# Kernel optimization log

Measured on AMD Instinct MI355X. Metric: run time of the kernel, lower is better.

The kernel has to match this reference:

```python
import jax, jax.numpy as jnp
import numpy as np

B, S, D = 4, 2048, 1024
E = 8
DFF = 4096
CAP_FACTOR = 1.25


def setup_inputs() -> dict:
    key = jax.random.key(0)
    ks = jax.random.split(key, 4)
    std_gate = float(np.sqrt(0.1 / D))
    inputs = jax.random.normal(ks[0], (B, S, D), dtype=jnp.float32)
    gate_w = jax.random.normal(ks[1], (E, D), dtype=jnp.float32) * std_gate
    w1 = jax.random.normal(ks[2], (E, D, DFF), dtype=jnp.float32) * (1.0 / np.sqrt(D))
    b1 = jnp.zeros((E, DFF), dtype=jnp.float32)
    w2 = jax.random.normal(ks[3], (E, DFF, D), dtype=jnp.float32) * (1.0 / np.sqrt(DFF))
    b2 = jnp.zeros((E, D), dtype=jnp.float32)
    return {"inputs": inputs, "gate_w": gate_w, "w1": w1, "b1": b1, "w2": w2, "b2": b2}


def reference(inputs, gate_w, w1, b1, w2, b2):
    d_model = inputs.shape[-1]
    tokens = inputs.reshape(-1, d_model)            # [T, D]
    T = tokens.shape[0]
    num_experts = gate_w.shape[0]
    capacity = int(np.ceil(CAP_FACTOR * T / num_experts))

    # fp32 gate (FP32LinearGate): logits = tokens @ gate_w.T
    logits = jnp.einsum('td,ed->te', tokens.astype(jnp.float32), gate_w)
    probs = jax.nn.softmax(logits, axis=-1)         # [T, E]

    # Top-1 routing with capacity
    expert_idx = jnp.argmax(probs, axis=-1)         # [T]
    mask = jax.nn.one_hot(expert_idx, num_experts, dtype=jnp.float32)  # [T, E]
    ranks = jnp.cumsum(mask, axis=0) - 1.0          # position of each token within its expert
    keep = (ranks < capacity) * mask                # drop tokens over capacity, [T, E]
    pos = ranks.astype(jnp.int32)                   # [T, E]
    # sec_mask: [T, E, C] one-hot placement of kept tokens into capacity slots
    sec_mask = jax.nn.one_hot(pos, capacity, dtype=jnp.float32) * keep[:, :, None]
    combine_weights = probs[:, :, None] * sec_mask  # [T, E, C]

    # Dispatch: dense matmul against routing mask (fallback path of MoeLayer)
    dispatch = jnp.einsum('tec,td->ecd', sec_mask, tokens)  # [E, C, D]

    # Grouped expert FFN
    h = jax.nn.relu(jnp.einsum('ecd,edh->ech', dispatch, w1) + b1[:, None, :])
    expert_out = jnp.einsum('ech,ehd->ecd', h, w2) + b2[:, None, :]  # [E, C, D]

    # Combine
    ans = jnp.einsum('tec,ecd->td', combine_weights, expert_out)
    return ans.reshape(inputs.shape)
```

## Files before the change

kernel.cpp:

```cpp
#include <hip/hip_runtime.h>
#include <hip/hip_bf16.h>

#define TOKENS 8192
#define DMODEL 1024
#define NEXP   8
#define DFF    4096
#define CAP    1280

typedef short bf16x8_t __attribute__((ext_vector_type(8)));
typedef float f32x4_t  __attribute__((ext_vector_type(4)));

__device__ __forceinline__ float bf2f(ushort u) {
    union { unsigned int i; float f; } v; v.i = ((unsigned int)u) << 16; return v.f;
}
__device__ __forceinline__ ushort f2bf(float f) {
    union { float f; unsigned int i; } v; v.f = f;
    unsigned int r = v.i + 0x7fffu + ((v.i >> 16) & 1u);
    return (ushort)(r >> 16);
}
__device__ __forceinline__ void load_lds16(const void* g, void* l) {
    __builtin_amdgcn_global_load_lds(
        (const __attribute__((address_space(1))) void*)g,
        (__attribute__((address_space(3))) void*)l, 16, 0, 0);
}

__global__ __launch_bounds__(256) void gate_kernel(
    const float* __restrict__ tokens, const float* __restrict__ gw,
    int* __restrict__ eidx, float* __restrict__ prob)
{
    int lane = threadIdx.x & 63;
    int wave = threadIdx.x >> 6;
    int t = blockIdx.x * 4 + wave;
    const float* tok = tokens + (long)t * DMODEL;
    float s[NEXP] = {0.f,0.f,0.f,0.f,0.f,0.f,0.f,0.f};
    #pragma unroll
    for (int c = 0; c < 4; c++) {
        int d = c * 256 + lane * 4;
        float4 x = *(const float4*)(tok + d);
        #pragma unroll
        for (int e = 0; e < NEXP; e++) {
            float4 g = *(const float4*)(gw + e * DMODEL + d);
            s[e] += x.x*g.x + x.y*g.y + x.z*g.z + x.w*g.w;
        }
    }
    #pragma unroll
    for (int e = 0; e < NEXP; e++) {
        #pragma unroll
        for (int off = 32; off > 0; off >>= 1) s[e] += __shfl_xor(s[e], off);
    }
    if (lane == 0) {
        float m = s[0]; int am = 0;
        #pragma unroll
        for (int e = 1; e < NEXP; e++) if (s[e] > m) { m = s[e]; am = e; }
        float sum = 0.f;
        #pragma unroll
        for (int e = 0; e < NEXP; e++) sum += expf(s[e] - m);
        eidx[t] = am;
        prob[t] = 1.0f / sum;
    }
}

__global__ __launch_bounds__(256) void route_scan(
    const int* __restrict__ eidx, int* __restrict__ pos)
{
    __shared__ int hist[256][NEXP];
    int tid = threadIdx.x;
    int base = tid * 32;
    #pragma unroll
    for (int e = 0; e < NEXP; e++) hist[tid][e] = 0;
    for (int i = 0; i < 32; i++) hist[tid][eidx[base + i]]++;
    __syncthreads();
    if (tid < NEXP) {
        int run = 0;
        for (int i = 0; i < 256; i++) { int v = hist[i][tid]; hist[i][tid] = run; run += v; }
    }
    __syncthreads();
    for (int i = 0; i < 32; i++) {
        int e = eidx[base + i];
        pos[base + i] = hist[tid][e]++;
    }
}

__global__ __launch_bounds__(256) void dispatch_gather(
    const float* __restrict__ tokens, const int* __restrict__ eidx,
    const int* __restrict__ pos, ushort* __restrict__ disp)
{
    int t = blockIdx.x;
    int p = pos[t];
    if (p >= CAP) return;
    int e = eidx[t];
    int d = threadIdx.x * 4;
    float4 v = *(const float4*)(tokens + (long)t * DMODEL + d);
    union { uint2 u; ushort h[4]; } o;
    o.h[0] = f2bf(v.x); o.h[1] = f2bf(v.y); o.h[2] = f2bf(v.z); o.h[3] = f2bf(v.w);
    *(uint2*)(disp + ((long)e * CAP + p) * DMODEL + d) = o.u;
}

__global__ __launch_bounds__(256) void transpose_f32_bf16(
    const float* __restrict__ in, ushort* __restrict__ out, int R, int C)
{
    __shared__ ushort tile[64][72];
    long base = (long)blockIdx.z * R * C;
    int r0 = blockIdx.y * 64, c0 = blockIdx.x * 64;
    int tid = threadIdx.x;
    int rr = tid >> 2;
    int cc = (tid & 3) * 16;
    const float* ip = in + base + (long)(r0 + rr) * C + (c0 + cc);
    #pragma unroll
    for (int q = 0; q < 4; q++) {
        float4 v = *(const float4*)(ip + q * 4);
        tile[cc + q*4 + 0][rr] = f2bf(v.x);
        tile[cc + q*4 + 1][rr] = f2bf(v.y);
        tile[cc + q*4 + 2][rr] = f2bf(v.z);
        tile[cc + q*4 + 3][rr] = f2bf(v.w);
    }
    __syncthreads();
    ushort* op = out + base + (long)(c0 + rr) * R + (r0 + cc);
    *(uint4*)op       = *(const uint4*)&tile[rr][cc];
    *(uint4*)(op + 8) = *(const uint4*)&tile[rr][cc + 8];
}

__global__ __launch_bounds__(256) void gemm_bt(
    const ushort* __restrict__ A, const ushort* __restrict__ B,
    const float* __restrict__ bias, ushort* __restrict__ C,
    int M, int N, int K, int do_relu,
    long sA, long sB, long sBias, long sC)
{
    A += blockIdx.z * sA; B += blockIdx.z * sB;
    bias += blockIdx.z * sBias; C += blockIdx.z * sC;

    __shared__ ushort As[128 * 64];
    __shared__ ushort Bs[128 * 64];

    int tid  = threadIdx.x;
    int lane = tid & 63, wave = tid >> 6;
    int wm = (wave >> 1) * 64, wn = (wave & 1) * 64;
    int fm = lane & 15;
    int q  = lane >> 4;
    int rx = fm & 7;
    int m0 = blockIdx.y * 128, n0 = blockIdx.x * 128;

    int srow = lane >> 3;
    int schk = (lane & 7) ^ srow;
    const ushort* Ag = A + (long)(m0 + 32*wave + srow) * K + schk * 8;
    const ushort* Bg = B + (long)(n0 + 32*wave + srow) * K + schk * 8;
    ushort* AsW = &As[(32*wave) * 64];
    ushort* BsW = &Bs[(32*wave) * 64];

    f32x4_t acc[4][4];
    #pragma unroll
    for (int i = 0; i < 4; i++)
        #pragma unroll
        for (int j = 0; j < 4; j++) acc[i][j] = (f32x4_t){0.f,0.f,0.f,0.f};

    for (int k0 = 0; k0 < K; k0 += 64) {
        #pragma unroll
        for (int t = 0; t < 4; t++) {
            load_lds16(Ag + (long)(8*t) * K + k0, AsW + (8*t) * 64);
            load_lds16(Bg + (long)(8*t) * K + k0, BsW + (8*t) * 64);
        }
        __syncthreads();
        #pragma unroll
        for (int kk = 0; kk < 64; kk += 32) {
            int l0 = (kk >> 3) + q;
            bf16x8_t af[4], bf[4];
            #pragma unroll
            for (int i = 0; i < 4; i++) {
                int r = wm + 16*i + fm;
                af[i] = *(const bf16x8_t*)&As[r * 64 + (l0 ^ rx) * 8];
            }
            #pragma unroll
            for (int j = 0; j < 4; j++) {
                int r = wn + 16*j + fm;
                bf[j] = *(const bf16x8_t*)&Bs[r * 64 + (l0 ^ rx) * 8];
            }
            #pragma unroll
            for (int i = 0; i < 4; i++)
                #pragma unroll
                for (int j = 0; j < 4; j++)
                    acc[i][j] = __builtin_amdgcn_mfma_f32_16x16x32_bf16(af[i], bf[j], acc[i][j], 0, 0, 0);
        }
        __syncthreads();
    }

    #pragma unroll
    for (int j = 0; j < 4; j++) {
        int col = n0 + wn + 16*j + fm;
        float bv = bias[col];
        #pragma unroll
        for (int i = 0; i < 4; i++) {
            int row = m0 + wm + 16*i + q * 4;
            #pragma unroll
            for (int r = 0; r < 4; r++) {
                float v = acc[i][j][r] + bv;
                if (do_relu) v = fmaxf(v, 0.f);
                C[(long)(row + r) * N + col] = f2bf(v);
            }
        }
    }
}

__global__ __launch_bounds__(256) void combine_kernel(
    const ushort* __restrict__ eo, const int* __restrict__ eidx,
    const int* __restrict__ pos, const float* __restrict__ prob,
    float* __restrict__ out)
{
    int t = blockIdx.x;
    int p = pos[t];
    int d = threadIdx.x * 4;
    float4 o;
    if (p < CAP) {
        int e = eidx[t];
        float w = prob[t];
        union { uint2 u; ushort h[4]; } v;
        v.u = *(const uint2*)(eo + ((long)e * CAP + p) * DMODEL + d);
        o.x = w * bf2f(v.h[0]);
        o.y = w * bf2f(v.h[1]);
        o.z = w * bf2f(v.h[2]);
        o.w = w * bf2f(v.h[3]);
    } else {
        o = (float4){0.f, 0.f, 0.f, 0.f};
    }
    *(float4*)(out + (long)t * DMODEL + d) = o;
}

extern "C" void kernel_launch(void* const* d_in, const int* in_sizes, int n_in,
                              void* d_out, int out_size, void* d_ws, size_t ws_size,
                              hipStream_t stream) {
    const float* tokens = (const float*)d_in[0];
    const float* gate_w = (const float*)d_in[1];
    const float* w1     = (const float*)d_in[2];
    const float* b1     = (const float*)d_in[3];
    const float* w2     = (const float*)d_in[4];
    const float* b2     = (const float*)d_in[5];
    float* outp = (float*)d_out;

    char* w = (char*)d_ws;
    ushort* w1T  = (ushort*)w; w += (size_t)NEXP * DFF * DMODEL * 2;
    ushort* w2T  = (ushort*)w; w += (size_t)NEXP * DMODEL * DFF * 2;
    ushort* disp = (ushort*)w; w += (size_t)NEXP * CAP * DMODEL * 2;
    ushort* h    = (ushort*)w; w += (size_t)NEXP * CAP * DFF * 2;
    ushort* eo   = (ushort*)w; w += (size_t)NEXP * CAP * DMODEL * 2;
    int*   eidx  = (int*)w;   w += TOKENS * 4;
    int*   pos   = (int*)w;   w += TOKENS * 4;
    float* prob  = (float*)w; w += TOKENS * 4;

    transpose_f32_bf16<<<dim3(DFF/64, DMODEL/64, NEXP), 256, 0, stream>>>(w1, w1T, DMODEL, DFF);
    transpose_f32_bf16<<<dim3(DMODEL/64, DFF/64, NEXP), 256, 0, stream>>>(w2, w2T, DFF, DMODEL);

    gate_kernel<<<TOKENS/4, 256, 0, stream>>>(tokens, gate_w, eidx, prob);
    route_scan<<<1, 256, 0, stream>>>(eidx, pos);
    dispatch_gather<<<TOKENS, 256, 0, stream>>>(tokens, eidx, pos, disp);

    gemm_bt<<<dim3(DFF/128, CAP/128, NEXP), 256, 0, stream>>>(
        disp, w1T, b1, h, CAP, DFF, DMODEL, 1,
        (long)CAP*DMODEL, (long)DFF*DMODEL, DFF, (long)CAP*DFF);
    gemm_bt<<<dim3(DMODEL/128, CAP/128, NEXP), 256, 0, stream>>>(
        h, w2T, b2, eo, CAP, DMODEL, DFF, 0,
        (long)CAP*DFF, (long)DMODEL*DFF, DMODEL, (long)CAP*DMODEL);

    combine_kernel<<<TOKENS, 256, 0, stream>>>(eo, eidx, pos, prob, outp);
}
```

Measured before the change: 584.2 us.

## Rewrite expert GEMM with 256x256 double-buffered tiles and workgroup swizzle

Replaces the 128x128 single-buffered grouped GEMM with a 256x256 tile, 512-thread kernel that double-buffers LDS, prefetches the next K-tile while computing in four phases with fine-grained vmcnt waits, and raises wave priority around MFMA blocks. It also remaps workgroup IDs in an XCD-aware swizzle for better L2 locality. The larger tile raises arithmetic intensity and reduces global traffic. In exchange it uses 128 KB of LDS and many accumulator registers, which limits occupancy. The grids also shrink (e.g. 4x5x8 for the second GEMM), which may underfill the CUs and leave a tail.

```diff
diff --git a/kernel.cpp b/kernel.cpp
--- a/kernel.cpp
+++ b/kernel.cpp
@@ -120,81 +120,136 @@
     *(uint4*)(op + 8) = *(const uint4*)&tile[rr][cc + 8];
 }
 
-__global__ __launch_bounds__(256) void gemm_bt(
+#define BM 256
+#define BN 256
+#define BK 64
+#define TILE_E (BM*BK)
+
+__global__ __launch_bounds__(512, 2) void gemm_bt256(
     const ushort* __restrict__ A, const ushort* __restrict__ B,
     const float* __restrict__ bias, ushort* __restrict__ C,
-    int M, int N, int K, int do_relu,
+    int N, int K, int do_relu,
     long sA, long sB, long sBias, long sC)
 {
-    A += blockIdx.z * sA; B += blockIdx.z * sB;
-    bias += blockIdx.z * sBias; C += blockIdx.z * sC;
-
-    __shared__ ushort As[128 * 64];
-    __shared__ ushort Bs[128 * 64];
+    __shared__ ushort As[2*TILE_E];
+    __shared__ ushort Bs[2*TILE_E];
+
+    int gx = gridDim.x, gy = gridDim.y;
+    int nwg = gx * gy * gridDim.z;
+    int lin = blockIdx.x + gx * (blockIdx.y + gy * blockIdx.z);
+    int cpx = nwg >> 3;
+    int swz = (lin & 7) * cpx + (lin >> 3);
+    int bz  = swz / (gx * gy);
+    int rem = swz - bz * gx * gy;
+    int by  = rem / gx, bx = rem - by * gx;
+
+    A += bz * sA; B += bz * sB; bias += bz * sBias; C += bz * sC;
+    long m0 = (long)by * BM, n0 = (long)bx * BN;
 
     int tid  = threadIdx.x;
     int lane = tid & 63, wave = tid >> 6;
-    int wm = (wave >> 1) * 64, wn = (wave & 1) * 64;
+    int wm = (wave >> 2) * 128;
+    int wn = (wave & 3) * 64;
     int fm = lane & 15;
     int q  = lane >> 4;
     int rx = fm & 7;
-    int m0 = blockIdx.y * 128, n0 = blockIdx.x * 128;
-
-    int srow = lane >> 3;
-    int schk = (lane & 7) ^ srow;
-    const ushort* Ag = A + (long)(m0 + 32*wave + srow) * K + schk * 8;
-    const ushort* Bg = B + (long)(n0 + 32*wave + srow) * K + schk * 8;
-    ushort* AsW = &As[(32*wave) * 64];
-    ushort* BsW = &Bs[(32*wave) * 64];
-
-    f32x4_t acc[4][4];
-    #pragma unroll
-    for (int i = 0; i < 4; i++)
+
+    int rl   = wave * 8 + (lane >> 3);
+    int loff = ((lane & 7) ^ (lane >> 3)) * 8;
+    const ushort* Ag = A + (m0 + rl) * (long)K + loff;
+    const ushort* Bg = B + (n0 + rl) * (long)K + loff;
+
+    f32x4_t acc[8][4];
+    #pragma unroll
+    for (int i = 0; i < 8; i++)
         #pragma unroll
         for (int j = 0; j < 4; j++) acc[i][j] = (f32x4_t){0.f,0.f,0.f,0.f};
 
-    for (int k0 = 0; k0 < K; k0 += 64) {
-        #pragma unroll
-        for (int t = 0; t < 4; t++) {
-            load_lds16(Ag + (long)(8*t) * K + k0, AsW + (8*t) * 64);
-            load_lds16(Bg + (long)(8*t) * K + k0, BsW + (8*t) * 64);
+    int KT = K >> 6;
+
+    {
+        ushort* Ad = As; ushort* Bd = Bs;
+        #pragma unroll
+        for (int s = 0; s < 4; s++)
+            load_lds16(Bg + (long)(64*s) * K, Bd + s*4096 + wave*512);
+        load_lds16(Ag,                 Ad + 0*4096 + wave*512);
+        load_lds16(Ag + (long)128*K,   Ad + 2*4096 + wave*512);
+        load_lds16(Ag + (long) 64*K,   Ad + 1*4096 + wave*512);
+        load_lds16(Ag + (long)192*K,   Ad + 3*4096 + wave*512);
+        asm volatile("s_waitcnt vmcnt(0)" ::: "memory");
+        __builtin_amdgcn_s_barrier();
+    }
+
+    for (int kt = 0; kt < KT; ++kt) {
+        const ushort* Asb = As + (kt & 1) * TILE_E;
+        const ushort* Bsb = Bs + (kt & 1) * TILE_E;
+        bf16x8_t bf[4][2];
+        #pragma unroll
+        for (int ph = 0; ph < 4; ++ph) {
+            if (ph == 0) {
+                #pragma unroll
+                for (int j = 0; j < 4; j++) {
+                    int r = wn + 16*j + fm;
+                    #pragma unroll
+                    for (int kk = 0; kk < 2; kk++)
+                        bf[j][kk] = *(const bf16x8_t*)&Bsb[r*64 + (((kk<<2)+q) ^ rx)*8];
+                }
+            }
+            bf16x8_t af[2][2];
+            #pragma unroll
+            for (int i2 = 0; i2 < 2; i2++) {
+                int r = wm + 16*(2*ph + i2) + fm;
+                #pragma unroll
+                for (int kk = 0; kk < 2; kk++)
+                    af[i2][kk] = *(const bf16x8_t*)&Asb[r*64 + (((kk<<2)+q) ^ rx)*8];
+            }
+            if (ph == 0 && kt + 1 < KT) {
+                long k0 = (long)(kt + 1) * 64;
+                ushort* Ad = As + ((kt + 1) & 1) * TILE_E;
+                ushort* Bd = Bs + ((kt + 1) & 1) * TILE_E;
+                #pragma unroll
+                for (int s = 0; s < 4; s++)
+                    load_lds16(Bg + (long)(64*s)*K + k0, Bd + s*4096 + wave*512);
+                load_lds16(Ag + k0,                Ad + 0*4096 + wave*512);
+                load_lds16(Ag + (long)128*K + k0,  Ad + 2*4096 + wave*512);
+                asm volatile("" ::: "memory");
+                __builtin_amdgcn_sched_barrier(0);
+                load_lds16(Ag + (long) 64*K + k0,  Ad + 1*4096 + wave*512);
+                load_lds16(Ag + (long)192*K + k0,  Ad + 3*4096 + wave*512);
+            }
+            __builtin_amdgcn_s_barrier();
+            __builtin_amdgcn_s_setprio(1);
+            #pragma unroll
+            for (int kk = 0; kk < 2; kk++)
+                #pragma unroll
+                for (int i2 = 0; i2 < 2; i2++)
+                    #pragma unroll
+                    for (int j = 0; j < 4; j++)
+                        acc[2*ph + i2][j] = __builtin_amdgcn_mfma_f32_16x16x32_bf16(
+                            af[i2][kk], bf[j][kk], acc[2*ph + i2][j], 0, 0, 0);
+            __builtin_amdgcn_s_setprio(0);
+            if (ph == 1) {
+                if (kt + 1 < KT) asm volatile("s_waitcnt vmcnt(8)" ::: "memory");
+                else             asm volatile("s_waitcnt vmcnt(0)" ::: "memory");
+            }
+            if (ph == 3 && kt + 1 < KT)
+                asm volatile("s_waitcnt vmcnt(2)" ::: "memory");
+            __builtin_amdgcn_s_barrier();
         }
-        __syncthreads();
-        #pragma unroll
-        for (int kk = 0; kk < 64; kk += 32) {
-            int l0 = (kk >> 3) + q;
-            bf16x8_t af[4], bf[4];
-            #pragma unroll
-            for (int i = 0; i < 4; i++) {
-                int r = wm + 16*i + fm;
-                af[i] = *(const bf16x8_t*)&As[r * 64 + (l0 ^ rx) * 8];
-            }
-            #pragma unroll
-            for (int j = 0; j < 4; j++) {
-                int r = wn + 16*j + fm;
-                bf[j] = *(const bf16x8_t*)&Bs[r * 64 + (l0 ^ rx) * 8];
-            }
-            #pragma unroll
-            for (int i = 0; i < 4; i++)
-                #pragma unroll
-                for (int j = 0; j < 4; j++)
-                    acc[i][j] = __builtin_amdgcn_mfma_f32_16x16x32_bf16(af[i], bf[j], acc[i][j], 0, 0, 0);
-        }
-        __syncthreads();
     }
 
     #pragma unroll
     for (int j = 0; j < 4; j++) {
-        int col = n0 + wn + 16*j + fm;
+        long col = n0 + wn + 16*j + fm;
         float bv = bias[col];
         #pragma unroll
-        for (int i = 0; i < 4; i++) {
-            int row = m0 + wm + 16*i + q * 4;
+        for (int i = 0; i < 8; i++) {
+            long row = m0 + wm + 16*i + q * 4;
             #pragma unroll
             for (int r = 0; r < 4; r++) {
                 float v = acc[i][j][r] + bv;
                 if (do_relu) v = fmaxf(v, 0.f);
-                C[(long)(row + r) * N + col] = f2bf(v);
+                C[(row + r) * N + col] = f2bf(v);
             }
         }
     }
@@ -252,11 +307,11 @@
     route_scan<<<1, 256, 0, stream>>>(eidx, pos);
     dispatch_gather<<<TOKENS, 256, 0, stream>>>(tokens, eidx, pos, disp);
 
-    gemm_bt<<<dim3(DFF/128, CAP/128, NEXP), 256, 0, stream>>>(
-        disp, w1T, b1, h, CAP, DFF, DMODEL, 1,
+    gemm_bt256<<<dim3(DFF/BN, CAP/BM, NEXP), 512, 0, stream>>>(
+        disp, w1T, b1, h, DFF, DMODEL, 1,
         (long)CAP*DMODEL, (long)DFF*DMODEL, DFF, (long)CAP*DFF);
-    gemm_bt<<<dim3(DMODEL/128, CAP/128, NEXP), 256, 0, stream>>>(
-        h, w2T, b2, eo, CAP, DMODEL, DFF, 0,
+    gemm_bt256<<<dim3(DMODEL/BN, CAP/BM, NEXP), 512, 0, stream>>>(
+        h, w2T, b2, eo, DMODEL, DFF, 0,
         (long)CAP*DFF, (long)DMODEL*DFF, DMODEL, (long)CAP*DMODEL);
 
     combine_kernel<<<TOKENS, 256, 0, stream>>>(eo, eidx, pos, prob, outp);
```

After: 658.8 us. 1.13x slower.

## Parallelize routing scan with packed wave prefix sums; swizzle transpose LDS tile

Applied to the files above, without the earlier changes.

The single-block routing scan now uses 1024 threads, each handling 8 tokens. Per-expert counts are packed as 16-bit fields into two 64-bit words, so a wave-level shuffle prefix sum plus a small cross-wave scan computes positions. This replaces the serial 256-step per-expert scan done by only 8 threads. Separately, the weight transpose kernel now uses coalesced row loads and an XOR-swizzled LDS layout to avoid bank conflicts on the scattered bf16 writes, and stores 16-byte rows on output.

```diff
diff --git a/kernel.cpp b/kernel.cpp
--- a/kernel.cpp
+++ b/kernel.cpp
@@ -60,25 +60,55 @@
     }
 }
 
-__global__ __launch_bounds__(256) void route_scan(
+__global__ __launch_bounds__(1024) void route_scan(
     const int* __restrict__ eidx, int* __restrict__ pos)
 {
-    __shared__ int hist[256][NEXP];
+    __shared__ unsigned long long pa[16], pb[16];
     int tid = threadIdx.x;
-    int base = tid * 32;
-    #pragma unroll
-    for (int e = 0; e < NEXP; e++) hist[tid][e] = 0;
-    for (int i = 0; i < 32; i++) hist[tid][eidx[base + i]]++;
+    int lane = tid & 63, wid = tid >> 6;
+    int4 e0 = *(const int4*)(eidx + tid * 8);
+    int4 e1 = *(const int4*)(eidx + tid * 8 + 4);
+    int le[8] = {e0.x, e0.y, e0.z, e0.w, e1.x, e1.y, e1.z, e1.w};
+    unsigned long long ha = 0, hb = 0;
+    #pragma unroll
+    for (int i = 0; i < 8; i++) {
+        int e = le[i];
+        if (e < 4) ha += 1ull << (e * 16);
+        else       hb += 1ull << ((e - 4) * 16);
+    }
+    unsigned long long ia = ha, ib = hb;
+    #pragma unroll
+    for (int off = 1; off < 64; off <<= 1) {
+        unsigned long long ua = __shfl_up(ia, off);
+        unsigned long long ub = __shfl_up(ib, off);
+        if (lane >= off) { ia += ua; ib += ub; }
+    }
+    if (lane == 63) { pa[wid] = ia; pb[wid] = ib; }
     __syncthreads();
-    if (tid < NEXP) {
-        int run = 0;
-        for (int i = 0; i < 256; i++) { int v = hist[i][tid]; hist[i][tid] = run; run += v; }
+    if (tid < 64) {
+        unsigned long long va = (lane < 16) ? pa[lane] : 0;
+        unsigned long long vb = (lane < 16) ? pb[lane] : 0;
+        unsigned long long oa = va, ob = vb;
+        #pragma unroll
+        for (int off = 1; off < 16; off <<= 1) {
+            unsigned long long ua = __shfl_up(va, off);
+            unsigned long long ub = __shfl_up(vb, off);
+            if (lane >= off) { va += ua; vb += ub; }
+        }
+        if (lane < 16) { pa[lane] = va - oa; pb[lane] = vb - ob; }
     }
     __syncthreads();
-    for (int i = 0; i < 32; i++) {
-        int e = eidx[base + i];
-        pos[base + i] = hist[tid][e]++;
-    }
+    unsigned long long ba = pa[wid] + (ia - ha);
+    unsigned long long bb = pb[wid] + (ib - hb);
+    int po[8];
+    #pragma unroll
+    for (int i = 0; i < 8; i++) {
+        int e = le[i];
+        if (e < 4) { int sh = e * 16;       po[i] = (int)((ba >> sh) & 0xffffu); ba += 1ull << sh; }
+        else       { int sh = (e - 4) * 16; po[i] = (int)((bb >> sh) & 0xffffu); bb += 1ull << sh; }
+    }
+    *(int4*)(pos + tid * 8)     = (int4){po[0], po[1], po[2], po[3]};
+    *(int4*)(pos + tid * 8 + 4) = (int4){po[4], po[5], po[6], po[7]};
 }
 
 __global__ __launch_bounds__(256) void dispatch_gather(
@@ -99,25 +129,32 @@
 __global__ __launch_bounds__(256) void transpose_f32_bf16(
     const float* __restrict__ in, ushort* __restrict__ out, int R, int C)
 {
-    __shared__ ushort tile[64][72];
+    __shared__ ushort tile[64 * 64];
     long base = (long)blockIdx.z * R * C;
     int r0 = blockIdx.y * 64, c0 = blockIdx.x * 64;
     int tid = threadIdx.x;
-    int rr = tid >> 2;
-    int cc = (tid & 3) * 16;
-    const float* ip = in + base + (long)(r0 + rr) * C + (c0 + cc);
+    int rr = tid >> 4;
+    int cf = (tid & 15) * 4;
+    const float* ip = in + base + (long)(r0 + rr) * C + c0 + cf;
     #pragma unroll
     for (int q = 0; q < 4; q++) {
-        float4 v = *(const float4*)(ip + q * 4);
-        tile[cc + q*4 + 0][rr] = f2bf(v.x);
-        tile[cc + q*4 + 1][rr] = f2bf(v.y);
-        tile[cc + q*4 + 2][rr] = f2bf(v.z);
-        tile[cc + q*4 + 3][rr] = f2bf(v.w);
+        int r = rr + q * 16;
+        float4 v = *(const float4*)(ip + (long)q * 16 * C);
+        int rlo = r & 7, rhi = r >> 3;
+        tile[(cf+0) * 64 + ((rhi ^ ((cf+0) & 7)) << 3) + rlo] = f2bf(v.x);
+        tile[(cf+1) * 64 + ((rhi ^ ((cf+1) & 7)) << 3) + rlo] = f2bf(v.y);
+        tile[(cf+2) * 64 + ((rhi ^ ((cf+2) & 7)) << 3) + rlo] = f2bf(v.z);
+        tile[(cf+3) * 64 + ((rhi ^ ((cf+3) & 7)) << 3) + rlo] = f2bf(v.w);
     }
     __syncthreads();
-    ushort* op = out + base + (long)(c0 + rr) * R + (r0 + cc);
-    *(uint4*)op       = *(const uint4*)&tile[rr][cc];
-    *(uint4*)(op + 8) = *(const uint4*)&tile[rr][cc + 8];
+    int oc = tid >> 3;
+    int j  = tid & 7;
+    #pragma unroll
+    for (int q = 0; q < 2; q++) {
+        int c = oc + q * 32;
+        uint4 w = *(const uint4*)&tile[c * 64 + ((j ^ (c & 7)) << 3)];
+        *(uint4*)(out + base + (long)(c0 + c) * R + r0 + j * 8) = w;
+    }
 }
 
 __global__ __launch_bounds__(256) void gemm_bt(
@@ -249,7 +286,7 @@
     transpose_f32_bf16<<<dim3(DMODEL/64, DFF/64, NEXP), 256, 0, stream>>>(w2, w2T, DFF, DMODEL);
 
     gate_kernel<<<TOKENS/4, 256, 0, stream>>>(tokens, gate_w, eidx, prob);
-    route_scan<<<1, 256, 0, stream>>>(eidx, pos);
+    route_scan<<<1, 1024, 0, stream>>>(eidx, pos);
     dispatch_gather<<<TOKENS, 256, 0, stream>>>(tokens, eidx, pos, disp);
 
     gemm_bt<<<dim3(DFF/128, CAP/128, NEXP), 256, 0, stream>>>(
```

Measured after the change: 581.9 us. No clear change (-0.4%).
